# Kernel tuning notes

Hardware: AMD Instinct MI355X
Metric: run time of the kernel (lower is better)

Reference implementation:

```python
import jax, jax.numpy as jnp
import numpy as np

EPS = 1e-7  # keras backend epsilon
B, D_IN, H, L, DEPTH = 16384, 784, 512, 32, 2

def _lrelu(x):
    return jax.nn.leaky_relu(x, 0.3)  # tf.keras LeakyReLU default alpha

def _router(h, W1, b1, W2, b2, W3, b3):
    h = _lrelu(h @ W1 + b1)
    h = _lrelu(h @ W2 + b2)
    return jax.nn.sigmoid((h @ W3 + b3)[:, 0])

def setup_inputs():
    key = jax.random.key(0)
    ks = jax.random.split(key, 20)
    s = 0.02
    n = lambda k, sh: jax.random.normal(k, sh, jnp.float32) * s
    return {
        'x': jax.random.uniform(ks[0], (B, D_IN), jnp.float32),
        'enc_W0': n(ks[1], (D_IN, H)), 'enc_b0': jnp.zeros((H,), jnp.float32),
        'enc_W': n(ks[2], (3, H, H)), 'enc_b': jnp.zeros((3, H), jnp.float32),
        'dense_Wmu': n(ks[3], (7, H, L)), 'dense_bmu': jnp.zeros((7, L), jnp.float32),
        'dense_Wsig': n(ks[4], (7, H, L)), 'dense_bsig': jnp.zeros((7, L), jnp.float32),
        'trans_Wh': n(ks[5], (6, L, H)), 'trans_bh': jnp.zeros((6, H), jnp.float32),
        'trans_Wmu': n(ks[6], (6, H, L)), 'trans_bmu': jnp.zeros((6, L), jnp.float32),
        'trans_Wsig': n(ks[7], (6, H, L)), 'trans_bsig': jnp.zeros((6, L), jnp.float32),
        'routp_W1': n(ks[8], (3, L, H)), 'routp_b1': jnp.zeros((3, H), jnp.float32),
        'routp_W2': n(ks[9], (3, H, H)), 'routp_b2': jnp.zeros((3, H), jnp.float32),
        'routp_W3': n(ks[10], (3, H, 1)), 'routp_b3': jnp.zeros((3, 1), jnp.float32),
        'routq_W1': n(ks[11], (3, H, H)), 'routq_b1': jnp.zeros((3, H), jnp.float32),
        'routq_W2': n(ks[12], (3, H, H)), 'routq_b2': jnp.zeros((3, H), jnp.float32),
        'routq_W3': n(ks[13], (3, H, 1)), 'routq_b3': jnp.zeros((3, 1), jnp.float32),
        'dec_W1': n(ks[14], (4, L, H)), 'dec_b1': jnp.zeros((4, H), jnp.float32),
        'dec_W2': n(ks[15], (4, H, D_IN)), 'dec_b2': jnp.zeros((4, D_IN), jnp.float32),
    }

def reference(x, enc_W0, enc_b0, enc_W, enc_b,
              dense_Wmu, dense_bmu, dense_Wsig, dense_bsig,
              trans_Wh, trans_bh, trans_Wmu, trans_bmu, trans_Wsig, trans_bsig,
              routp_W1, routp_b1, routp_W2, routp_b2, routp_W3, routp_b3,
              routq_W1, routq_b1, routq_W2, routq_b2, routq_W3, routq_b3,
              dec_W1, dec_b1, dec_W2, dec_b2):
    Bn = x.shape[0]
    # bottom-up encoder chain; encoders collects layers i >= len - (depth+1) = 1
    d = _lrelu(x @ enc_W0 + enc_b0)
    encoders = []
    for i in range(3):
        d = _lrelu(d @ enc_W[i] + enc_b[i])
        encoders.append(d)
    depth_of = [0, 1, 1, 2, 2, 2, 2]  # BFS depth of the 7 tree nodes
    probs = {0: jnp.ones((Bn,), x.dtype)}
    zs = {}
    kl_nodes_tot = jnp.zeros((Bn,), x.dtype)
    kl_dec_tot = jnp.zeros((Bn,), x.dtype)
    kl_root = None
    leaves_prob, recons = [], []
    base = jax.random.key(1)
    for k in range(7):
        dl = depth_of[k]
        d = encoders[DEPTH - dl]
        mu_q_hat = d @ dense_Wmu[k] + dense_bmu[k]
        sig_q_hat = jax.nn.softplus(d @ dense_Wsig[k] + dense_bsig[k])
        if k == 0:
            mu_p = jnp.zeros_like(mu_q_hat)
            sig_p = jnp.ones_like(sig_q_hat)
            mu_q, sig_q = mu_q_hat, sig_q_hat
        else:
            zp = zs[(k - 1) // 2]
            h = _lrelu(zp @ trans_Wh[k - 1] + trans_bh[k - 1])
            mu_p = h @ trans_Wmu[k - 1] + trans_bmu[k - 1]
            sig_p = jax.nn.softplus(h @ trans_Wsig[k - 1] + trans_bsig[k - 1])
            # compute_posterior: precision-weighted fusion
            sig_q = 1.0 / (1.0 / sig_q_hat + 1.0 / sig_p)
            mu_q = sig_q * (mu_q_hat / sig_q_hat + mu_p / sig_p)
        vq = sig_q + EPS
        vp = sig_p + EPS
        # KL(N(mu_q, vq) || N(mu_p, vp)) for diag Gaussians (scale = sqrt(sigma+eps))
        kl = 0.5 * jnp.sum(vq / vp + (mu_q - mu_p) ** 2 / vp - 1.0 + jnp.log(vp / vq), axis=1)
        kl_node = jnp.clip(probs[k] * kl, -1.0, 1000.0)
        if k == 0:
            kl_root = kl_node
        else:
            kl_nodes_tot = kl_nodes_tot + kl_node
        eps_n = jax.random.normal(jax.random.fold_in(base, k), mu_q.shape, x.dtype)
        z = mu_q + jnp.sqrt(vq) * eps_n  # reparameterized sample
        zs[k] = z
        if k < 3:  # internal node: routing
            pl = _router(z, routp_W1[k], routp_b1[k], routp_W2[k], routp_b2[k], routp_W3[k], routp_b3[k])
            plq = _router(d, routq_W1[k], routq_b1[k], routq_W2[k], routq_b2[k], routq_W3[k], routq_b3[k])
            kl_dec = plq * jnp.log(EPS + plq / (pl + EPS)) + (1.0 - plq) * jnp.log(EPS + (1.0 - plq) / (1.0 - pl + EPS))
            kl_dec_tot = kl_dec_tot + probs[k] * kl_dec
            probs[2 * k + 1] = probs[k] * plq
            probs[2 * k + 2] = probs[k] * (1.0 - plq)
        else:  # leaf: decode
            leaves_prob.append(probs[k])
            h = _lrelu(z @ dec_W1[k - 3] + dec_b1[k - 3])
            recons.append(jax.nn.sigmoid(h @ dec_W2[k - 3] + dec_b2[k - 3]))
    rec_losses = jnp.zeros((Bn,), x.dtype)
    for p, r in zip(leaves_prob, recons):
        bce = -jnp.sum(x * jnp.log(r + EPS) + (1.0 - x) * jnp.log(1.0 - r + EPS), axis=1)
        rec_losses = rec_losses + p * bce
    # elbo_samples, per-sample total loss (shape [B])
    return kl_nodes_tot + kl_dec_tot + kl_root + rec_losses
```

## Files before the change

kernel.cpp:

```cpp
#include <hip/hip_runtime.h>
#include <cstdint>
#include <cstddef>

#define B_ROWS 16384
#define DIN 784
#define HD 512
#define LD 32
#define BMT 64

typedef __attribute__((ext_vector_type(8))) short short8;
typedef __attribute__((ext_vector_type(4))) float f32x4;
typedef __attribute__((ext_vector_type(4))) unsigned short us4;

struct I4 { int x, y, z, w; };
__device__ inline int i4get(I4 v, int z) { return z == 0 ? v.x : z == 1 ? v.y : z == 2 ? v.z : v.w; }

__device__ inline unsigned short f2bf(float v) {
  union { float f; unsigned u; } x; x.f = v;
  unsigned r = x.u + 0x7fffu + ((x.u >> 16) & 1u);
  return (unsigned short)(r >> 16);
}
__device__ inline float bf2f(unsigned short b) {
  union { unsigned u; float f; } x; x.u = ((unsigned)b) << 16;
  return x.f;
}

__host__ __device__ inline void threefry2x32(uint32_t k0, uint32_t k1,
                                             uint32_t x0, uint32_t x1,
                                             uint32_t& o0, uint32_t& o1) {
  uint32_t ks2 = k0 ^ k1 ^ 0x1BD11BDAu;
#define TF_ROT(x, d) (((x) << (d)) | ((x) >> (32 - (d))))
#define TF_R(r) { x0 += x1; x1 = TF_ROT(x1, r); x1 ^= x0; }
  x0 += k0; x1 += k1;
  TF_R(13) TF_R(15) TF_R(26) TF_R(6)
  x0 += k1; x1 += ks2 + 1u;
  TF_R(17) TF_R(29) TF_R(16) TF_R(24)
  x0 += ks2; x1 += k0 + 2u;
  TF_R(13) TF_R(15) TF_R(26) TF_R(6)
  x0 += k0; x1 += k1 + 3u;
  TF_R(17) TF_R(29) TF_R(16) TF_R(24)
  x0 += k1; x1 += ks2 + 4u;
  TF_R(13) TF_R(15) TF_R(26) TF_R(6)
  x0 += ks2; x1 += k0 + 5u;
  o0 = x0; o1 = x1;
#undef TF_R
#undef TF_ROT
}

__device__ inline float erfinv_f(float x) {
  float w = -log1pf(-x * x);
  float p;
  if (w < 5.0f) {
    w -= 2.5f;
    p = 2.81022636e-08f;
    p = fmaf(p, w, 3.43273939e-07f);
    p = fmaf(p, w, -3.5233877e-06f);
    p = fmaf(p, w, -4.39150654e-06f);
    p = fmaf(p, w, 0.00021858087f);
    p = fmaf(p, w, -0.00125372503f);
    p = fmaf(p, w, -0.00417768164f);
    p = fmaf(p, w, 0.246640727f);
    p = fmaf(p, w, 1.50140941f);
  } else {
    w = sqrtf(w) - 3.0f;
    p = -0.000200214257f;
    p = fmaf(p, w, 0.000100950558f);
    p = fmaf(p, w, 0.00134934322f);
    p = fmaf(p, w, -0.00367342844f);
    p = fmaf(p, w, 0.00573950773f);
    p = fmaf(p, w, -0.0076224613f);
    p = fmaf(p, w, 0.00943887047f);
    p = fmaf(p, w, 1.00167406f);
    p = fmaf(p, w, 2.83297682f);
  }
  return p * x;
}

__device__ inline float jax_normal_elem(uint32_t ka, uint32_t kb, uint32_t idx) {
  uint32_t b1, b2;
  threefry2x32(ka, kb, 0u, idx, b1, b2);
  uint32_t bits = b1 ^ b2;
  uint32_t fb = (bits >> 9) | 0x3f800000u;
  float f = __uint_as_float(fb) - 1.0f;
  const float lo = -0.99999994f;
  float u = f * 2.0f + lo;
  u = fmaxf(u, lo);
  return 1.41421356f * erfinv_f(u);
}

struct WJob {
  unsigned short pi;
  unsigned src_off, dst_off, start;
  short K, N, Np, Kp;
};
struct WJobs { WJob j[56]; unsigned total; };

constexpr WJobs make_jobs() {
  WJobs W{};
  int idx = 0; unsigned start = 0; unsigned d = 0;
  auto add = [&](int pi, unsigned so, int K, int N, int Np, int Kp, unsigned doff) {
    W.j[idx].pi = (unsigned short)pi; W.j[idx].src_off = so; W.j[idx].dst_off = doff;
    W.j[idx].start = start; W.j[idx].K = (short)K; W.j[idx].N = (short)N;
    W.j[idx].Np = (short)Np; W.j[idx].Kp = (short)Kp;
    start += (unsigned)(Np * Kp); ++idx;
  };
  add(0, 0, 784, 512, 512, 800, d); d += 512 * 800;
  for (int i = 0; i < 3; ++i) { add(1, i * 262144u, 512, 512, 512, 512, d); d += 262144; }
  for (int k = 0; k < 7; ++k) { add(2, k * 16384u, 512, 32, 32, 512, d);
                                add(3, k * 16384u, 512, 32, 32, 512, d + 16384); d += 32768; }
  for (int i = 0; i < 6; ++i) { add(4, i * 16384u, 32, 512, 512, 32, d); d += 16384; }
  for (int i = 0; i < 6; ++i) { add(5, i * 16384u, 512, 32, 32, 512, d);
                                add(6, i * 16384u, 512, 32, 32, 512, d + 16384); d += 32768; }
  for (int k = 0; k < 3; ++k) { add(7, k * 16384u, 32, 512, 512, 32, d); d += 16384; }
  for (int k = 0; k < 3; ++k) { add(8, k * 262144u, 512, 512, 512, 512, d); d += 262144; }
  for (int k = 0; k < 3; ++k) { add(9, k * 262144u, 512, 512, 512, 512, d); d += 262144; }
  for (int k = 0; k < 3; ++k) { add(10, k * 262144u, 512, 512, 512, 512, d); d += 262144; }
  for (int i = 0; i < 4; ++i) { add(11, i * 16384u, 32, 512, 512, 32, d); d += 16384; }
  for (int i = 0; i < 4; ++i) { add(12, i * 401408u, 512, 784, 896, 512, d); d += 458752; }
  W.total = start;
  return W;
}
__device__ constexpr WJobs g_jobs = make_jobs();

struct TileTable { unsigned ts[57]; };
constexpr TileTable make_tiles() {
  TileTable T{}; WJobs J = make_jobs();
  unsigned acc = 0;
  for (int i = 0; i < 56; ++i) {
    T.ts[i] = acc;
    acc += (unsigned)(J.j[i].Np / 32) * (unsigned)(J.j[i].Kp / 32);
  }
  T.ts[56] = acc;
  return T;
}
__device__ constexpr TileTable g_tiles = make_tiles();

#define OFF_ENC0T 0u
#define OFF_ENCT 409600u
#define OFF_DENSE 1196032u
#define OFF_TWH 1425408u
#define OFF_TMS 1523712u
#define OFF_RP1 1720320u
#define OFF_RP2 1769472u
#define OFF_RQ1 2555904u
#define OFF_RQ2 3342336u
#define OFF_DC1 4128768u
#define OFF_DC2 4194304u
#define ARENA_ELEMS 6029312u

struct WSrcs { const float* p[13]; };

__global__ void wconv_k(WSrcs srcs, unsigned short* __restrict__ arena) {
  __shared__ unsigned short tile[32][34];
  unsigned bid = blockIdx.x;
  int jo = 0;
#pragma unroll 1
  while (jo + 1 < 56 && g_tiles.ts[jo + 1] <= bid) ++jo;
  const WJob J = g_jobs.j[jo];
  unsigned t = bid - g_tiles.ts[jo];
  unsigned ktiles = (unsigned)J.Kp / 32u;
  unsigned n0 = (t / ktiles) * 32u, k0 = (t % ktiles) * 32u;
  int ty = threadIdx.x >> 3, tx4 = (threadIdx.x & 7) * 4;
  float v0 = 0, v1 = 0, v2 = 0, v3 = 0;
  int kk = (int)k0 + ty;
  if (kk < J.K) {
    const float* sp = srcs.p[J.pi] + J.src_off + (size_t)kk * J.N + n0 + tx4;
    int nb = (int)(n0 + tx4);
    if (nb + 3 < J.N) {
      float4 v = *reinterpret_cast<const float4*>(sp);
      v0 = v.x; v1 = v.y; v2 = v.z; v3 = v.w;
    } else {
      if (nb + 0 < J.N) v0 = sp[0];
      if (nb + 1 < J.N) v1 = sp[1];
      if (nb + 2 < J.N) v2 = sp[2];
      if (nb + 3 < J.N) v3 = sp[3];
    }
  }
  tile[tx4 + 0][ty] = f2bf(v0);
  tile[tx4 + 1][ty] = f2bf(v1);
  tile[tx4 + 2][ty] = f2bf(v2);
  tile[tx4 + 3][ty] = f2bf(v3);
  __syncthreads();
  us4 w;
  w.x = tile[ty][tx4 + 0]; w.y = tile[ty][tx4 + 1];
  w.z = tile[ty][tx4 + 2]; w.w = tile[ty][tx4 + 3];
  *reinterpret_cast<us4*>(&arena[J.dst_off + (size_t)(n0 + ty) * J.Kp + k0 + tx4]) = w;
}

__global__ void xconv_k(const float* __restrict__ x, unsigned short* __restrict__ xb800,
                        unsigned short* __restrict__ xb784) {
  unsigned g = blockIdx.x * 256u + threadIdx.x;
  unsigned r = g / 200u, c4 = g % 200u;
  unsigned c = c4 * 4u;
  float v0 = 0, v1 = 0, v2 = 0, v3 = 0;
  if (c + 3 < 784u) {
    float4 v = *reinterpret_cast<const float4*>(x + (size_t)r * 784u + c);
    v0 = v.x; v1 = v.y; v2 = v.z; v3 = v.w;
  } else {
    if (c + 0 < 784u) v0 = x[(size_t)r * 784u + c + 0];
    if (c + 1 < 784u) v1 = x[(size_t)r * 784u + c + 1];
    if (c + 2 < 784u) v2 = x[(size_t)r * 784u + c + 2];
    if (c + 3 < 784u) v3 = x[(size_t)r * 784u + c + 3];
  }
  us4 w; w.x = f2bf(v0); w.y = f2bf(v1); w.z = f2bf(v2); w.w = f2bf(v3);
  *reinterpret_cast<us4*>(&xb800[(size_t)r * 800u + c]) = w;
  if (c + 3 < 784u)
    *reinterpret_cast<us4*>(&xb784[(size_t)r * 784u + c]) = w;
}

template <int BM, int BN, int ACT, typename OT>
__global__ void mgemm_k(const unsigned short* __restrict__ A, int sA,
                        const unsigned short* __restrict__ Wt,
                        const float* __restrict__ b1, const float* __restrict__ b2,
                        OT* __restrict__ C, int sC, int Nreal, int K,
                        I4 zAo, I4 zWo, I4 zCo, int zB1, int zB2,
                        const unsigned short* __restrict__ xx) {
  constexpr int BK = 32;
  constexpr int WN = BN / 2;
  constexpr int NF = WN / 16;
  constexpr int MR = BM / 32;
  __shared__ unsigned short As[BM][BK];
  __shared__ unsigned short Bs[BN][BK];
  __shared__ float sums[BM][2];
  const int z = blockIdx.z;
  A += i4get(zAo, z);
  Wt += i4get(zWo, z);
  C += i4get(zCo, z);
  b1 += (size_t)z * zB1;
  if (ACT == 3 || ACT == 4) { if (b2) b2 += (size_t)z * zB2; }

  const int tid = threadIdx.x;
  const int lane = tid & 63;
  const int wid = tid >> 6;
  const int wr = wid >> 1, wc = wid & 1;
  const int bm = blockIdx.x * BM;
  const int bn = blockIdx.y * BN;
  const int lr = lane >> 2;
  const int lk = (lane & 3) * 8;

  f32x4 acc[MR][NF];
#pragma unroll
  for (int m = 0; m < MR; ++m)
#pragma unroll
    for (int n = 0; n < NF; ++n) acc[m][n] = (f32x4){0.f, 0.f, 0.f, 0.f};

  const int ar = wr * (BM / 2) + (lane & 15);
  const int ac = (lane >> 4) * 8;
  const int br = wc * WN + (lane & 15);

  for (int k0 = 0; k0 < K; k0 += BK) {
    constexpr int CA = BM / 16;
#pragma unroll
    for (int cc = 0; cc < CA / 4; ++cc) {
      int c = wid * (CA / 4) + cc;
      const unsigned short* g = A + (size_t)(bm + c * 16 + lr) * sA + k0 + lk;
      __builtin_amdgcn_global_load_lds(
          (const __attribute__((address_space(1))) void*)g,
          (__attribute__((address_space(3))) void*)(&As[c * 16][0]), 16, 0, 0);
    }
    constexpr int CB = BN / 16;
#pragma unroll
    for (int cc = 0; cc < CB / 4; ++cc) {
      int c = wid * (CB / 4) + cc;
      const unsigned short* g = Wt + (size_t)(bn + c * 16 + lr) * K + k0 + lk;
      __builtin_amdgcn_global_load_lds(
          (const __attribute__((address_space(1))) void*)g,
          (__attribute__((address_space(3))) void*)(&Bs[c * 16][0]), 16, 0, 0);
    }
    __syncthreads();

    short8 aF[MR], bF[NF];
#pragma unroll
    for (int m = 0; m < MR; ++m)
      aF[m] = *reinterpret_cast<const short8*>(&As[ar + m * 16][ac]);
#pragma unroll
    for (int n = 0; n < NF; ++n)
      bF[n] = *reinterpret_cast<const short8*>(&Bs[br + n * 16][ac]);
#pragma unroll
    for (int m = 0; m < MR; ++m)
#pragma unroll
      for (int n = 0; n < NF; ++n)
        acc[m][n] = __builtin_amdgcn_mfma_f32_16x16x32_bf16(aF[m], bF[n], acc[m][n], 0, 0, 0);
    __syncthreads();
  }

  if constexpr (ACT == 4 || ACT == 5) {
    const int row0 = bm + wr * (BM / 2) + (lane >> 4) * 4;
#pragma unroll
    for (int m = 0; m < MR; ++m) {
#pragma unroll
      for (int r = 0; r < 4; ++r) {
        float s = 0.0f;
        int grow = row0 + m * 16 + r;
#pragma unroll
        for (int n = 0; n < NF; ++n) {
          int col = bn + wc * WN + n * 16 + (lane & 15);
          float v = acc[m][n][r];
          if constexpr (ACT == 4) {
            v += b1[col];
            v = (v >= 0.0f) ? v : 0.3f * v;
            s += v * b2[col];
          } else {
            if (col < Nreal) {
              v += b1[col];
              float sg = 1.0f / (1.0f + expf(-v));
              float xv = bf2f(xx[(size_t)grow * Nreal + col]);
              s += xv * logf(sg + 1e-7f) + (1.0f - xv) * logf(1.0f - sg + 1e-7f);
            }
          }
        }
#pragma unroll
        for (int msk = 1; msk < 16; msk <<= 1) s += __shfl_xor(s, msk, 64);
        if ((lane & 15) == 0) sums[wr * (BM / 2) + m * 16 + (lane >> 4) * 4 + r][wc] = s;
      }
    }
    __syncthreads();
    if (tid < BM) {
      float* Cf = (float*)C;
      Cf[(size_t)(bm + tid) * sC + blockIdx.y] = sums[tid][0] + sums[tid][1];
    }
  } else {
#pragma unroll
    for (int m = 0; m < MR; ++m) {
      int row = bm + wr * (BM / 2) + m * 16 + (lane >> 4) * 4;
#pragma unroll
      for (int n = 0; n < NF; ++n) {
        int col = bn + wc * WN + n * 16 + (lane & 15);
        if (col < Nreal) {
#pragma unroll
          for (int r = 0; r < 4; ++r) {
            float v = acc[m][n][r];
            if constexpr (ACT == 3) {
              int nl = col >> 6, cin = col & 63;
              if (cin < 32) {
                v += b1[nl * 32 + cin];
              } else {
                v += b2[nl * 32 + (cin - 32)];
                v = fmaxf(v, 0.0f) + log1pf(expf(-fabsf(v)));
              }
            } else {
              v += b1[col];
              if (ACT == 1) v = (v >= 0.0f) ? v : 0.3f * v;
            }
            size_t oidx = (size_t)(row + r) * sC + col;
            if constexpr (sizeof(OT) == 2) C[oidx] = (OT)f2bf(v);
            else C[oidx] = (OT)v;
          }
        }
      }
    }
  }
}

struct Keys { uint32_t a[7]; uint32_t b[7]; };

__global__ void node_k(int kstart, Keys keys,
                       const float* __restrict__ musigAll,
                       const float* __restrict__ mupsigAll,
                       const float* __restrict__ probs,
                       unsigned short* __restrict__ zbuf,
                       float* __restrict__ contrib) {
  const int knode = kstart + blockIdx.y;
  const int row = blockIdx.x * 8 + (threadIdx.x >> 5);
  const int j = threadIdx.x & 31;
  const float* mq = musigAll + (size_t)row * 448 + 64 * knode;
  float mqh = mq[j], sqh = mq[32 + j];
  float mu_q, sig_q, mu_p, sig_p;
  if (knode == 0) {
    mu_p = 0.0f; sig_p = 1.0f; mu_q = mqh; sig_q = sqh;
  } else {
    const float* mp = mupsigAll + (size_t)row * 448 + 64 * knode;
    mu_p = mp[j]; sig_p = mp[32 + j];
    sig_q = 1.0f / (1.0f / sqh + 1.0f / sig_p);
    mu_q = sig_q * (mqh / sqh + mu_p / sig_p);
  }
  float vq = sig_q + 1e-7f, vp = sig_p + 1e-7f;
  float dm = mu_q - mu_p;
  float kj = vq / vp + dm * dm / vp - 1.0f + logf(vp / vq);
#pragma unroll
  for (int msk = 1; msk < 32; msk <<= 1) kj += __shfl_xor(kj, msk, 64);
  float e = jax_normal_elem(keys.a[knode], keys.b[knode], (uint32_t)(row * 32 + j));
  zbuf[(size_t)knode * B_ROWS * 32 + (size_t)row * 32 + j] = f2bf(mu_q + sqrtf(vq) * e);
  if (j == 0) {
    float p = (knode == 0) ? 1.0f : probs[(size_t)knode * B_ROWS + row];
    float kn = fminf(fmaxf(p * 0.5f * kj, -1.0f), 1000.0f);
    contrib[(size_t)knode * B_ROWS + row] = kn;
  }
}

__global__ void route_k(int kstart, const float* __restrict__ plp,
                        const float* __restrict__ plqp,
                        const float* __restrict__ rpb3, const float* __restrict__ rqb3,
                        float* __restrict__ probs, float* __restrict__ contrib) {
  const int k = kstart + blockIdx.y;
  const int row = blockIdx.x * 256 + threadIdx.x;
  const float* pp = plp + ((size_t)k * B_ROWS + row) * 4;
  const float* pq = plqp + ((size_t)k * B_ROWS + row) * 4;
  float sl = pp[0] + pp[1] + pp[2] + pp[3];
  float sq = pq[0] + pq[1] + pq[2] + pq[3];
  float pl = 1.0f / (1.0f + expf(-(sl + rpb3[k])));
  float plq = 1.0f / (1.0f + expf(-(sq + rqb3[k])));
  float p = (k == 0) ? 1.0f : probs[(size_t)k * B_ROWS + row];
  float kld = plq * logf(1e-7f + plq / (pl + 1e-7f)) +
              (1.0f - plq) * logf(1e-7f + (1.0f - plq) / (1.0f - pl + 1e-7f));
  contrib[(size_t)(7 + k) * B_ROWS + row] = p * kld;
  probs[(size_t)(2 * k + 1) * B_ROWS + row] = p * plq;
  probs[(size_t)(2 * k + 2) * B_ROWS + row] = p * (1.0f - plq);
}

__global__ void final_k(const float* __restrict__ contrib, const float* __restrict__ probs,
                        const float* __restrict__ pbce, float* __restrict__ out) {
  const int row = blockIdx.x * 256 + threadIdx.x;
  float s = 0.0f;
#pragma unroll
  for (int i = 0; i < 10; ++i) s += contrib[(size_t)i * B_ROWS + row];
#pragma unroll
  for (int l = 0; l < 4; ++l) {
    const float* pb = pbce + ((size_t)l * B_ROWS + row) * 7;
    float bs = 0.0f;
#pragma unroll
    for (int y = 0; y < 7; ++y) bs += pb[y];
    s += probs[(size_t)(3 + l) * B_ROWS + row] * (-bs);
  }
  out[row] = s;
}

extern "C" void kernel_launch(void* const* d_in, const int* in_sizes, int n_in,
                              void* d_out, int out_size, void* d_ws, size_t ws_size,
                              hipStream_t stream) {
  const float* x      = (const float*)d_in[0];
  const float* enc_W0 = (const float*)d_in[1];
  const float* enc_b0 = (const float*)d_in[2];
  const float* enc_W  = (const float*)d_in[3];
  const float* enc_b  = (const float*)d_in[4];
  const float* dWmu   = (const float*)d_in[5];
  const float* dbmu   = (const float*)d_in[6];
  const float* dWsig  = (const float*)d_in[7];
  const float* dbsig  = (const float*)d_in[8];
  const float* tWh    = (const float*)d_in[9];
  const float* tbh    = (const float*)d_in[10];
  const float* tWmu   = (const float*)d_in[11];
  const float* tbmu   = (const float*)d_in[12];
  const float* tWsig  = (const float*)d_in[13];
  const float* tbsig  = (const float*)d_in[14];
  const float* rpW1   = (const float*)d_in[15];
  const float* rpb1   = (const float*)d_in[16];
  const float* rpW2   = (const float*)d_in[17];
  const float* rpb2   = (const float*)d_in[18];
  const float* rpW3   = (const float*)d_in[19];
  const float* rpb3   = (const float*)d_in[20];
  const float* rqW1   = (const float*)d_in[21];
  const float* rqb1   = (const float*)d_in[22];
  const float* rqW2   = (const float*)d_in[23];
  const float* rqb2   = (const float*)d_in[24];
  const float* rqW3   = (const float*)d_in[25];
  const float* rqb3   = (const float*)d_in[26];
  const float* dcW1   = (const float*)d_in[27];
  const float* dcb1   = (const float*)d_in[28];
  const float* dcW2   = (const float*)d_in[29];
  const float* dcb2   = (const float*)d_in[30];
  float* out = (float*)d_out;
  (void)in_sizes; (void)n_in; (void)out_size; (void)ws_size;

  const size_t BR = B_ROWS;
  unsigned short* h = (unsigned short*)d_ws;
  unsigned short* encA  = h;
  unsigned short* encB  = h + BR * 512;
  unsigned short* encC  = h + BR * 1024;
  unsigned short* bufT  = h + BR * 1536;
  unsigned short* zbuf  = h + BR * 2560;
  unsigned short* xb784 = h + BR * 2784;
  unsigned short* arena = h + BR * 3568;
  size_t ho = BR * 3568 + ARENA_ELEMS;
  float* f = (float*)(h + ho);
  float* musigAll  = f;
  float* mupsigAll = f + BR * 448;
  float* probs     = f + BR * 896;
  float* plp       = f + BR * 903;
  float* plqp      = f + BR * 915;
  float* pbce      = f + BR * 927;
  float* contrib   = f + BR * 955;
  unsigned short* xb800 = (unsigned short*)f;

  const int offA = 0;
  const int offC = (int)(BR * 1024);
  const int offT = (int)(BR * 1536);

  Keys keys;
  for (int k = 0; k < 7; ++k) threefry2x32(0u, 1u, 0u, (uint32_t)k, keys.a[k], keys.b[k]);

  const I4 Z0 = {0, 0, 0, 0};
  constexpr TileTable HT = make_tiles();

  xconv_k<<<dim3((B_ROWS * 200) / 256), 256, 0, stream>>>(x, xb800, xb784);
  WSrcs srcs;
  srcs.p[0] = enc_W0; srcs.p[1] = enc_W; srcs.p[2] = dWmu; srcs.p[3] = dWsig;
  srcs.p[4] = tWh; srcs.p[5] = tWmu; srcs.p[6] = tWsig;
  srcs.p[7] = rpW1; srcs.p[8] = rpW2; srcs.p[9] = rqW1; srcs.p[10] = rqW2;
  srcs.p[11] = dcW1; srcs.p[12] = dcW2;
  wconv_k<<<dim3(HT.ts[56]), 256, 0, stream>>>(srcs, arena);

#define LAUNCH(BN, ACT, OT, A, sA, W, B1, B2, Cc, sC, Nr, K, gy, gz, zA, zW, zC, zb1, zb2, XX) \
  mgemm_k<BMT, BN, ACT, OT><<<dim3(B_ROWS / BMT, gy, gz), 256, 0, stream>>>( \
      A, sA, W, B1, B2, Cc, sC, Nr, K, zA, zW, zC, zb1, zb2, XX)

  LAUNCH(128, 1, unsigned short, xb800, 800, arena + OFF_ENC0T, enc_b0, nullptr,
         bufT, 512, 512, 800, 4, 1, Z0, Z0, Z0, 0, 0, nullptr);
  LAUNCH(128, 1, unsigned short, bufT, 512, arena + OFF_ENCT + 0u, enc_b + 0, nullptr,
         encA, 512, 512, 512, 4, 1, Z0, Z0, Z0, 0, 0, nullptr);
  LAUNCH(128, 3, float, encA, 512, arena + OFF_DENSE + 3u * 32768u, dbmu + 96, dbsig + 96,
         musigAll + 192, 448, 256, 512, 2, 1, Z0, Z0, Z0, 0, 0, nullptr);
  LAUNCH(128, 1, unsigned short, encA, 512, arena + OFF_ENCT + 262144u, enc_b + 512, nullptr,
         encB, 512, 512, 512, 4, 1, Z0, Z0, Z0, 0, 0, nullptr);
  LAUNCH(128, 3, float, encB, 512, arena + OFF_DENSE + 32768u, dbmu + 32, dbsig + 32,
         musigAll + 64, 448, 128, 512, 1, 1, Z0, Z0, Z0, 0, 0, nullptr);
  LAUNCH(128, 1, unsigned short, encB, 512, arena + OFF_ENCT + 524288u, enc_b + 1024, nullptr,
         encC, 512, 512, 512, 4, 1, Z0, Z0, Z0, 0, 0, nullptr);
  LAUNCH(64, 3, float, encC, 512, arena + OFF_DENSE, dbmu, dbsig,
         musigAll, 448, 64, 512, 1, 1, Z0, Z0, Z0, 0, 0, nullptr);
  LAUNCH(128, 1, unsigned short, encC, 512, arena + OFF_RQ1, rqb1, nullptr,
         bufT, 512, 512, 512, 4, 1, Z0, Z0, Z0, 0, 0, nullptr);
  {
    I4 zW = {0, 262144, 0, 0}, zC = {offA, offC, 0, 0};
    LAUNCH(128, 1, unsigned short, encB, 512, arena + OFF_RQ1 + 262144u, rqb1 + 512, nullptr,
           h, 512, 512, 512, 4, 2, Z0, zW, zC, 512, 0, nullptr);
  }
  {
    I4 zA = {offT, offA, offC, 0};
    I4 zW = {0, 262144, 524288, 0};
    I4 zC = {0, (int)(BR * 4), (int)(BR * 8), 0};
    LAUNCH(128, 4, float, h, 512, arena + OFF_RQ2, rqb2, rqW3,
           plqp, 4, 512, 512, 4, 3, zA, zW, zC, 512, 512, nullptr);
  }

  node_k<<<dim3(B_ROWS / 8, 1), 256, 0, stream>>>(0, keys, musigAll, mupsigAll, probs, zbuf, contrib);
  LAUNCH(128, 1, unsigned short, zbuf, 32, arena + OFF_RP1, rpb1, nullptr,
         bufT, 512, 512, 32, 4, 1, Z0, Z0, Z0, 0, 0, nullptr);
  LAUNCH(128, 4, float, bufT, 512, arena + OFF_RP2, rpb2, rpW3,
         plp, 4, 512, 512, 4, 1, Z0, Z0, Z0, 0, 0, nullptr);
  route_k<<<dim3(B_ROWS / 256, 1), 256, 0, stream>>>(0, plp, plqp, rpb3, rqb3, probs, contrib);

  LAUNCH(128, 1, unsigned short, zbuf, 32, arena + OFF_TWH, tbh, nullptr,
         bufT, 1024, 1024, 32, 8, 1, Z0, Z0, Z0, 0, 0, nullptr);
  {
    I4 zA = {0, 512, 0, 0}, zW = {0, 32768, 0, 0}, zC = {0, 64, 0, 0};
    LAUNCH(64, 3, float, bufT, 1024, arena + OFF_TMS, tbmu, tbsig,
           mupsigAll + 64, 448, 64, 512, 1, 2, zA, zW, zC, 32, 32, nullptr);
  }
  node_k<<<dim3(B_ROWS / 8, 2), 256, 0, stream>>>(1, keys, musigAll, mupsigAll, probs, zbuf, contrib);
  {
    I4 zA = {0, (int)(BR * 32), 0, 0}, zW = {0, 16384, 0, 0}, zC = {offA, offC, 0, 0};
    LAUNCH(128, 1, unsigned short, zbuf + BR * 32, 32, arena + OFF_RP1 + 16384u, rpb1 + 512, nullptr,
           h, 512, 512, 32, 4, 2, zA, zW, zC, 512, 0, nullptr);
    I4 zA2 = {offA, offC, 0, 0}, zW2 = {0, 262144, 0, 0}, zC2 = {0, (int)(BR * 4), 0, 0};
    LAUNCH(128, 4, float, h, 512, arena + OFF_RP2 + 262144u, rpb2 + 512, rpW3 + 512,
           plp + BR * 4, 4, 512, 512, 4, 2, zA2, zW2, zC2, 512, 512, nullptr);
  }
  route_k<<<dim3(B_ROWS / 256, 2), 256, 0, stream>>>(1, plp, plqp, rpb3, rqb3, probs, contrib);

  {
    I4 zA = {0, 512, 0, 0}, zW = {0, 32768, 0, 0}, zC = {0, 64, 0, 0};
    LAUNCH(128, 1, unsigned short, zbuf + BR * 32, 32, arena + OFF_TWH + 32768u, tbh + 1024, nullptr,
           bufT, 1024, 1024, 32, 8, 1, Z0, Z0, Z0, 0, 0, nullptr);
    LAUNCH(64, 3, float, bufT, 1024, arena + OFF_TMS + 65536u, tbmu + 64, tbsig + 64,
           mupsigAll + 192, 448, 64, 512, 1, 2, zA, zW, zC, 32, 32, nullptr);
    LAUNCH(128, 1, unsigned short, zbuf + BR * 64, 32, arena + OFF_TWH + 65536u, tbh + 2048, nullptr,
           bufT, 1024, 1024, 32, 8, 1, Z0, Z0, Z0, 0, 0, nullptr);
    LAUNCH(64, 3, float, bufT, 1024, arena + OFF_TMS + 131072u, tbmu + 128, tbsig + 128,
           mupsigAll + 320, 448, 64, 512, 1, 2, zA, zW, zC, 32, 32, nullptr);
  }
  node_k<<<dim3(B_ROWS / 8, 4), 256, 0, stream>>>(3, keys, musigAll, mupsigAll, probs, zbuf, contrib);

  {
    I4 zA1 = {0, (int)(BR * 32), 0, 0}, zW1 = {0, 16384, 0, 0}, zC1 = {0, (int)(BR * 512), 0, 0};
    I4 zA2 = {0, (int)(BR * 512), 0, 0}, zW2 = {0, 458752, 0, 0}, zC2 = {0, (int)(BR * 7), 0, 0};
    LAUNCH(128, 1, unsigned short, zbuf + BR * 96, 32, arena + OFF_DC1, dcb1, nullptr,
           bufT, 512, 512, 32, 4, 2, zA1, zW1, zC1, 512, 0, nullptr);
    LAUNCH(128, 5, float, bufT, 512, arena + OFF_DC2, dcb2, nullptr,
           pbce, 7, 784, 512, 7, 2, zA2, zW2, zC2, 784, 0, xb784);
    LAUNCH(128, 1, unsigned short, zbuf + BR * 160, 32, arena + OFF_DC1 + 32768u, dcb1 + 1024, nullptr,
           bufT, 512, 512, 32, 4, 2, zA1, zW1, zC1, 512, 0, nullptr);
    LAUNCH(128, 5, float, bufT, 512, arena + OFF_DC2 + 917504u, dcb2 + 1568, nullptr,
           pbce + BR * 14, 7, 784, 512, 7, 2, zA2, zW2, zC2, 784, 0, xb784);
  }

  final_k<<<dim3(B_ROWS / 256), 256, 0, stream>>>(contrib, probs, pbce, out);
#undef LAUNCH
}
```

Baseline: 669.5 us.

## Batch sibling transition and decoder GEMMs into wider z-grid launches, use fast math intrinsics

Merges the two level-2 transition hidden/mu-sigma GEMM pairs into one batched launch each, and the two decoder pairs into a single 4-way batched launch per stage, by using the z dimension of the grid with per-slice offsets into a larger h buffer. This cuts the number of kernel launches and gives each launch more blocks to fill the GPU. Separately, the BCE epilogue and softplus now use __expf/__logf instead of expf/logf, trading a little accuracy for cheaper transcendentals. The batched path needs enough space in h for 4x BR*512 or 2x BR*1024 elements.

```diff
diff --git a/kernel.cpp b/kernel.cpp
--- a/kernel.cpp
+++ b/kernel.cpp
@@ -303,9 +303,9 @@
           } else {
             if (col < Nreal) {
               v += b1[col];
-              float sg = 1.0f / (1.0f + expf(-v));
+              float sg = 1.0f / (1.0f + __expf(-v));
               float xv = bf2f(xx[(size_t)grow * Nreal + col]);
-              s += xv * logf(sg + 1e-7f) + (1.0f - xv) * logf(1.0f - sg + 1e-7f);
+              s += xv * __logf(sg + 1e-7f) + (1.0f - xv) * __logf(1.0f - sg + 1e-7f);
             }
           }
         }
@@ -336,7 +336,7 @@
                 v += b1[nl * 32 + cin];
               } else {
                 v += b2[nl * 32 + (cin - 32)];
-                v = fmaxf(v, 0.0f) + log1pf(expf(-fabsf(v)));
+                v = fmaxf(v, 0.0f) + log1pf(__expf(-fabsf(v)));
               }
             } else {
               v += b1[col];
@@ -559,29 +559,30 @@
   route_k<<<dim3(B_ROWS / 256, 2), 256, 0, stream>>>(1, plp, plqp, rpb3, rqb3, probs, contrib);
 
   {
-    I4 zA = {0, 512, 0, 0}, zW = {0, 32768, 0, 0}, zC = {0, 64, 0, 0};
+    I4 zA = {0, (int)(BR * 32), 0, 0};
+    I4 zW = {0, 32768, 0, 0};
+    I4 zC = {0, (int)(BR * 1024), 0, 0};
     LAUNCH(128, 1, unsigned short, zbuf + BR * 32, 32, arena + OFF_TWH + 32768u, tbh + 1024, nullptr,
-           bufT, 1024, 1024, 32, 8, 1, Z0, Z0, Z0, 0, 0, nullptr);
-    LAUNCH(64, 3, float, bufT, 1024, arena + OFF_TMS + 65536u, tbmu + 64, tbsig + 64,
-           mupsigAll + 192, 448, 64, 512, 1, 2, zA, zW, zC, 32, 32, nullptr);
-    LAUNCH(128, 1, unsigned short, zbuf + BR * 64, 32, arena + OFF_TWH + 65536u, tbh + 2048, nullptr,
-           bufT, 1024, 1024, 32, 8, 1, Z0, Z0, Z0, 0, 0, nullptr);
-    LAUNCH(64, 3, float, bufT, 1024, arena + OFF_TMS + 131072u, tbmu + 128, tbsig + 128,
-           mupsigAll + 320, 448, 64, 512, 1, 2, zA, zW, zC, 32, 32, nullptr);
+           h, 1024, 1024, 32, 8, 2, zA, zW, zC, 1024, 0, nullptr);
+    I4 zA2 = {0, 512, (int)(BR * 1024), (int)(BR * 1024 + 512)};
+    I4 zW2 = {0, 32768, 65536, 98304};
+    I4 zC2 = {0, 64, 128, 192};
+    LAUNCH(64, 3, float, h, 1024, arena + OFF_TMS + 65536u, tbmu + 64, tbsig + 64,
+           mupsigAll + 192, 448, 64, 512, 1, 4, zA2, zW2, zC2, 32, 32, nullptr);
   }
   node_k<<<dim3(B_ROWS / 8, 4), 256, 0, stream>>>(3, keys, musigAll, mupsigAll, probs, zbuf, contrib);
 
   {
-    I4 zA1 = {0, (int)(BR * 32), 0, 0}, zW1 = {0, 16384, 0, 0}, zC1 = {0, (int)(BR * 512), 0, 0};
-    I4 zA2 = {0, (int)(BR * 512), 0, 0}, zW2 = {0, 458752, 0, 0}, zC2 = {0, (int)(BR * 7), 0, 0};
+    I4 zA1 = {0, (int)(BR * 32), (int)(BR * 64), (int)(BR * 96)};
+    I4 zW1 = {0, 16384, 32768, 49152};
+    I4 zC1 = {0, (int)(BR * 512), (int)(BR * 1024), (int)(BR * 1536)};
     LAUNCH(128, 1, unsigned short, zbuf + BR * 96, 32, arena + OFF_DC1, dcb1, nullptr,
-           bufT, 512, 512, 32, 4, 2, zA1, zW1, zC1, 512, 0, nullptr);
-    LAUNCH(128, 5, float, bufT, 512, arena + OFF_DC2, dcb2, nullptr,
-           pbce, 7, 784, 512, 7, 2, zA2, zW2, zC2, 784, 0, xb784);
-    LAUNCH(128, 1, unsigned short, zbuf + BR * 160, 32, arena + OFF_DC1 + 32768u, dcb1 + 1024, nullptr,
-           bufT, 512, 512, 32, 4, 2, zA1, zW1, zC1, 512, 0, nullptr);
-    LAUNCH(128, 5, float, bufT, 512, arena + OFF_DC2 + 917504u, dcb2 + 1568, nullptr,
-           pbce + BR * 14, 7, 784, 512, 7, 2, zA2, zW2, zC2, 784, 0, xb784);
+           h, 512, 512, 32, 4, 4, zA1, zW1, zC1, 512, 0, nullptr);
+    I4 zA2 = {0, (int)(BR * 512), (int)(BR * 1024), (int)(BR * 1536)};
+    I4 zW2 = {0, 458752, 917504, 1376256};
+    I4 zC2 = {0, (int)(BR * 7), (int)(BR * 14), (int)(BR * 21)};
+    LAUNCH(128, 5, float, h, 512, arena + OFF_DC2, dcb2, nullptr,
+           pbce, 7, 784, 512, 7, 4, zA2, zW2, zC2, 784, 0, xb784);
   }
 
   final_k<<<dim3(B_ROWS / 256), 256, 0, stream>>>(contrib, probs, pbce, out);
```

New measurement: 621.7 us. -7.1%, faster.
